# Kernel tuning notes

Measured on AMD Instinct MI355X. Metric: run time of the kernel, lower is better.

The kernel has to match this reference:

```python
import jax, jax.numpy as jnp
import numpy as np

N, E, L, HID, HEADS, G = 50000, 800000, 2, 128, 8, 256
DK = HID // HEADS

def _ln(x, g, b, eps=1e-5):
    m = jnp.mean(x, axis=-1, keepdims=True)
    v = jnp.mean((x - m) ** 2, axis=-1, keepdims=True)
    return (x - m) * jax.lax.rsqrt(v + eps) * g + b

def setup_inputs() -> dict:
    key = jax.random.key(0)
    ks = jax.random.split(key, 24)
    rn = lambda i, s: (0.05 * jax.random.normal(ks[i], s)).astype(jnp.float32)
    return {
        'node_attr': jax.random.randint(ks[0], (N, 4), 0, 64, dtype=jnp.int32),
        'batch_idx': jnp.sort(jax.random.randint(ks[1], (N,), 0, G, dtype=jnp.int32)),
        'edge_index': jax.random.randint(ks[2], (2, E), 0, N, dtype=jnp.int32),
        'strat_dist': jax.random.randint(ks[3], (E,), 0, 32, dtype=jnp.int32),
        'strat_path': jax.random.randint(ks[4], (E,), 0, 16, dtype=jnp.int32),
        'atom_emb': rn(5, (4, 64, HID)),
        'dist_emb': rn(6, (L, 32, HID)),
        'path_emb': rn(7, (L, 16, HID)),
        'Wq': rn(8, (L, HID, HID)), 'bq': rn(9, (L, HID)),
        'Wk': rn(10, (L, HID, HID)), 'bk': rn(11, (L, HID)),
        'Wv': rn(12, (L, HID, HID)), 'bv': rn(13, (L, HID)),
        'Wa': rn(14, (L, HID, HID)), 'ba': rn(15, (L, HID)),
        'ln1_g': jnp.ones((L, HID), jnp.float32), 'ln1_b': jnp.zeros((L, HID), jnp.float32),
        'Wmid': rn(16, (L, HID, 2 * HID)), 'bmid': rn(17, (L, 2 * HID)),
        'Wo': rn(18, (L, 2 * HID, HID)), 'bo': rn(19, (L, HID)),
        'ln2_g': jnp.ones((L, HID), jnp.float32), 'ln2_b': jnp.zeros((L, HID), jnp.float32),
        'W_out': rn(20, (HID, 1)), 'b_out': jnp.zeros((1,), jnp.float32),
    }

def reference(node_attr, batch_idx, edge_index, strat_dist, strat_path,
              atom_emb, dist_emb, path_emb, Wq, bq, Wk, bk, Wv, bv, Wa, ba,
              ln1_g, ln1_b, Wmid, bmid, Wo, bo, ln2_g, ln2_b, W_out, b_out):
    # node encoder: sum of per-feature embeddings (AtomEncoder style)
    x = sum(atom_emb[f][node_attr[:, f]] for f in range(node_attr.shape[1]))  # [N, HID]
    src, tgt = edge_index[0], edge_index[1]  # j (source), i (target)
    inv_sqrt_dk = np.float32(1.0 / np.sqrt(DK))
    for l in range(L):
        # per-edge gather + relational encodings added to the source vector
        s = x[src] + dist_emb[l][strat_dist] + path_emb[l][strat_path]  # [E, HID]
        t = x[tgt]                                                      # [E, HID]
        q = (t @ Wq[l] + bq[l]).reshape(E, HEADS, DK)
        k = (s @ Wk[l] + bk[l]).reshape(E, HEADS, DK)
        v = (s @ Wv[l] + bv[l]).reshape(E, HEADS, DK)
        scores = jnp.sum(q * k, axis=-1) * inv_sqrt_dk  # [E, HEADS]
        # segment softmax keyed on target node id
        smax = jax.ops.segment_max(scores, tgt, num_segments=N)
        ex = jnp.exp(scores - smax[tgt])
        den = jax.ops.segment_sum(ex, tgt, num_segments=N)
        att = ex / (den[tgt] + 1e-16)                   # [E, HEADS]
        msg = (v * att[:, :, None]).reshape(E, HID)
        aggr = jax.ops.segment_sum(msg, tgt, num_segments=N)  # scatter-add
        # update: attn FFN + residual + LayerNorms (dropout is identity in eval)
        h = _ln(jax.nn.gelu(aggr, approximate=False) @ Wa[l] + ba[l] + x, ln1_g[l], ln1_b[l])
        h2 = jax.nn.gelu(h @ Wmid[l] + bmid[l], approximate=False) @ Wo[l] + bo[l]
        x = _ln(h2 + h, ln2_g[l], ln2_b[l])
    # global mean pool per graph, then readout
    cnt = jax.ops.segment_sum(jnp.ones((N,), x.dtype), batch_idx, num_segments=G)
    pooled = jax.ops.segment_sum(x, batch_idx, num_segments=G) / jnp.maximum(cnt, 1.0)[:, None]
    return pooled @ W_out + b_out
```

## Files before the change

### kernel.cpp

```cpp
#include <hip/hip_runtime.h>
#include <hip/hip_bf16.h>
#include <math.h>
#include <stdint.h>

#define N_NODES 50000
#define N_EDGES 800000
#define HID 128
#define NGRAPH 256
#define NLAYER 2
#define CAP 64

#define BIN_B 196
#define N_PAD (BIN_B * 256)

#define ENC_B 782
#define TKV_B 256
#define PREP1_B (BIN_B + ENC_B + TKV_B)

#define PREP0_B (132 + 782)

typedef __bf16 bf16x8 __attribute__((ext_vector_type(8)));
typedef __bf16 bf16x2 __attribute__((ext_vector_type(2)));
typedef float f32x4 __attribute__((ext_vector_type(4)));
typedef float f32x2 __attribute__((ext_vector_type(2)));

__device__ __forceinline__ float gelu_f(float v) {
    return 0.5f * v * (1.0f + erff(v * 0.70710678118654752f));
}

__device__ __forceinline__ f32x2 f8lo(uint32_t d) {
    return __builtin_amdgcn_cvt_pk_f32_fp8((int)d, false);
}
__device__ __forceinline__ f32x2 f8hi(uint32_t d) {
    return __builtin_amdgcn_cvt_pk_f32_fp8((int)d, true);
}
__device__ __forceinline__ uint32_t pk4_fp8(float a, float b, float c, float d) {
    int w = __builtin_amdgcn_cvt_pk_fp8_f32(a, b, 0, false);
    w = __builtin_amdgcn_cvt_pk_fp8_f32(c, d, w, true);
    return (uint32_t)w;
}
__device__ __forceinline__ f32x2 bfpair(uint32_t d) {
    f32x2 r;
    r[0] = __uint_as_float(d << 16);
    r[1] = __uint_as_float(d);
    return r;
}

__global__ __launch_bounds__(256) void prep0_kernel(
    const float* __restrict__ Wq, const float* __restrict__ Wa,
    const float* __restrict__ Wmid, const float* __restrict__ Wo,
    const float* __restrict__ Wk, const float* __restrict__ Wv,
    __bf16* __restrict__ wqkvf, __bf16* __restrict__ waf,
    __bf16* __restrict__ wmidf, __bf16* __restrict__ wof,
    const int* __restrict__ batch, const float* __restrict__ bout,
    const float* __restrict__ bq, const float* __restrict__ bk,
    const float* __restrict__ bv,
    float* __restrict__ invc, float* __restrict__ outp, float* __restrict__ bqkv,
    const int* __restrict__ src, const int* __restrict__ sd,
    const int* __restrict__ sp, uint32_t* __restrict__ pack) {
    int b = blockIdx.x;
    int tid = threadIdx.x;
    if (b < 128) {
        int u = b * 256 + tid;
        int l = u >> 14, r = u & 16383;
        const float* srcp;
        __bf16* dstp;
        int kg, scol, srcCO;
        if (r < 6144) {
            kg = r / 384;
            int uu = r % 384;
            int sec = uu >> 7, cc = uu & 127;
            scol = ((cc & 15) << 3) | (cc >> 4);
            const float* Ws = (sec == 0) ? Wq : (sec == 1) ? Wk : Wv;
            srcp = Ws + l * 16384;
            srcCO = 128;
            dstp = wqkvf + (size_t)l * 49152 + (size_t)r * 8;
        } else if (r < 8192) {
            int rr = r - 6144;
            kg = rr >> 7;
            int cc = rr & 127;
            scol = ((cc & 15) << 3) | (cc >> 4);
            srcp = Wa + l * 16384;
            srcCO = 128;
            dstp = waf + (size_t)l * 16384 + (size_t)rr * 8;
        } else if (r < 12288) {
            int rr = r - 8192;
            kg = rr >> 8;
            int uu = rr & 255;
            int blk = uu >> 7, cc = uu & 127;
            scol = blk * 128 + (((cc & 15) << 3) | (cc >> 4));
            srcp = Wmid + l * 32768;
            srcCO = 256;
            dstp = wmidf + (size_t)l * 32768 + (size_t)rr * 8;
        } else {
            int rr = r - 12288;
            kg = rr >> 7;
            int cc = rr & 127;
            scol = ((cc & 15) << 3) | (cc >> 4);
            srcp = Wo + l * 32768;
            srcCO = 128;
            dstp = wof + (size_t)l * 32768 + (size_t)rr * 8;
        }
        bf16x8 o;
#pragma unroll
        for (int j = 0; j < 8; j++) o[j] = (__bf16)srcp[(kg * 8 + j) * srcCO + scol];
        *(bf16x8*)dstp = o;
    } else if (b < 132) {
        int sb = b - 128;
        if (sb == 0) {
            int g = tid;
            int lo = 0, hi = N_NODES;
            while (lo < hi) { int mid = (lo + hi) >> 1; if (batch[mid] < g) lo = mid + 1; else hi = mid; }
            int start = lo;
            lo = start; hi = N_NODES;
            while (lo < hi) { int mid = (lo + hi) >> 1; if (batch[mid] < g + 1) lo = mid + 1; else hi = mid; }
            int c2 = lo - start;
            invc[g] = 1.0f / fmaxf((float)c2, 1.0f);
            outp[g] = bout[0];
        } else {
            int r = (sb - 1) * 256 + tid;
            int l = r / 384, c = r % 384;
            float v = (c < 128) ? bq[l * 128 + c]
                    : (c < 256) ? bk[l * 128 + c - 128]
                                : bv[l * 128 + c - 256];
            bqkv[r] = v;
        }
    } else {
        int e0 = (b - 132) * 1024 + tid * 4;
        if (e0 + 3 < N_EDGES) {
            int4 s4 = *(const int4*)(src + e0);
            int4 d4 = *(const int4*)(sd + e0);
            int4 p4 = *(const int4*)(sp + e0);
            uint4 o;
            o.x = (uint32_t)s4.x | ((uint32_t)((d4.x << 4) | p4.x) << 16);
            o.y = (uint32_t)s4.y | ((uint32_t)((d4.y << 4) | p4.y) << 16);
            o.z = (uint32_t)s4.z | ((uint32_t)((d4.z << 4) | p4.z) << 16);
            o.w = (uint32_t)s4.w | ((uint32_t)((d4.w << 4) | p4.w) << 16);
            *(uint4*)(pack + e0) = o;
        }
    }
}

__global__ __launch_bounds__(1024) void prep1_kernel(
    const int* __restrict__ attr, const float* __restrict__ aemb,
    __bf16* __restrict__ xb,
    const float* __restrict__ de, const float* __restrict__ pe,
    const float* __restrict__ Wk, const float* __restrict__ Wv,
    __bf16* __restrict__ tkv,
    const int* __restrict__ tgt, const uint32_t* __restrict__ pack,
    int* __restrict__ cnt, uint32_t* __restrict__ ei) {
    __shared__ int lcnt[256];
    __shared__ uint32_t lei[256 * CAP];
    __shared__ float sde[4][128];
    int b = blockIdx.x;
    int tid = threadIdx.x;
    if (b < BIN_B) {
        int lo = b << 8;
        if (tid < 256) lcnt[tid] = 0;
        __syncthreads();
        for (int it0 = 0; it0 < 192; it0 += 4) {
            int4 t4[4];
#pragma unroll
            for (int u = 0; u < 4; u++)
                t4[u] = *(const int4*)(tgt + (it0 + u) * 4096 + tid * 4);
#pragma unroll
            for (int u = 0; u < 4; u++) {
                int e0 = (it0 + u) * 4096 + tid * 4;
#pragma unroll
                for (int j = 0; j < 4; j++) {
                    int t = (j == 0) ? t4[u].x : (j == 1) ? t4[u].y : (j == 2) ? t4[u].z : t4[u].w;
                    unsigned tl = (unsigned)(t - lo);
                    if (tl < 256u) {
                        int r = atomicAdd(&lcnt[tl], 1);
                        if (r < CAP) lei[(tl << 6) + r] = pack[e0 + j];
                    }
                }
            }
        }
        for (int it = 192; it < 196; ++it) {
            int e0 = it * 4096 + tid * 4;
            if (e0 + 3 < N_EDGES) {
                int4 tg = *(const int4*)(tgt + e0);
#pragma unroll
                for (int j = 0; j < 4; j++) {
                    int t = (j == 0) ? tg.x : (j == 1) ? tg.y : (j == 2) ? tg.z : tg.w;
                    unsigned tl = (unsigned)(t - lo);
                    if (tl < 256u) {
                        int r = atomicAdd(&lcnt[tl], 1);
                        if (r < CAP) lei[(tl << 6) + r] = pack[e0 + j];
                    }
                }
            }
        }
        __syncthreads();
        if (tid < 256) {
            int t = lo + tid;
            if (t < N_NODES) cnt[t] = min(lcnt[tid], CAP);
        }
        uint32_t* gout = ei + ((size_t)lo << 6);
#pragma unroll
        for (int i2 = 0; i2 < 4; ++i2) {
            int w = i2 * 4096 + tid * 4;
            *(uint4*)(gout + w) = *(const uint4*)(lei + w);
        }
        return;
    }
    b -= BIN_B;
    if (b < ENC_B) {
        int gid = b * 1024 + tid;
        if (gid < N_NODES * 16) {
            int n = gid >> 4;
            int c8 = (gid & 15) << 3;
            const int4 a = *(const int4*)(attr + n * 4);
            const float* r0 = aemb + (size_t)(0 * 64 + a.x) * 128 + c8;
            const float* r1 = aemb + (size_t)(1 * 64 + a.y) * 128 + c8;
            const float* r2 = aemb + (size_t)(2 * 64 + a.z) * 128 + c8;
            const float* r3 = aemb + (size_t)(3 * 64 + a.w) * 128 + c8;
            f32x4 v0a = *(const f32x4*)r0, v0b = *(const f32x4*)(r0 + 4);
            f32x4 v1a = *(const f32x4*)r1, v1b = *(const f32x4*)(r1 + 4);
            f32x4 v2a = *(const f32x4*)r2, v2b = *(const f32x4*)(r2 + 4);
            f32x4 v3a = *(const f32x4*)r3, v3b = *(const f32x4*)(r3 + 4);
            bf16x8 o;
#pragma unroll
            for (int j = 0; j < 4; j++) {
                o[j] = (__bf16)(v0a[j] + v1a[j] + v2a[j] + v3a[j]);
                o[4 + j] = (__bf16)(v0b[j] + v1b[j] + v2b[j] + v3b[j]);
            }
            *(bf16x8*)(xb + (size_t)n * 128 + c8) = o;
        }
    } else {
        int bb = (b - ENC_B) * 4 + (tid >> 8);
        int c = tid & 255;
        int l = bb >> 9;
        int md = bb & 511;
        int dd = md >> 4, pp = md & 15;
        int g = tid >> 8;
        if (c < 128) sde[g][c] = de[l * 4096 + dd * 128 + c] + pe[l * 2048 + pp * 128 + c];
        __syncthreads();
        const float* W = (c < 128) ? (Wk + l * 16384) : (Wv + l * 16384);
        int cc = c & 127;
        float acc = 0.f;
#pragma unroll 4
        for (int k = 0; k < 128; k++) acc = fmaf(sde[g][k], W[k * 128 + cc], acc);
        tkv[(size_t)bb * 256 + c] = (__bf16)acc;
    }
}

__global__ __launch_bounds__(256) void qkv_gemm(
    const __bf16* __restrict__ A, const __bf16* __restrict__ Wf,
    const float* __restrict__ bias, __bf16* __restrict__ Qb,
    uint8_t* __restrict__ kv8, int M) {
    int tid = threadIdx.x;
    int bq = blockIdx.x;
    int sec = bq % 3;
    int rowblk = bq / 3;
    int lane = tid & 63;
    int wv = tid >> 6;
    int row0 = rowblk * 64 + wv * 16;
    int col0 = sec * 128;
    if (row0 >= M) return;
    int quad = lane >> 4, tq = lane & 15;
    f32x4 acc[8] = {};
#pragma unroll
    for (int k0 = 0; k0 < 128; k0 += 32) {
        int rr = row0 + tq;
        if (rr >= M) rr = M - 1;
        bf16x8 af = *(const bf16x8*)(A + (size_t)rr * 128 + k0 + quad * 8);
#pragma unroll
        for (int nt = 0; nt < 8; nt++) {
            bf16x8 bfr = *(const bf16x8*)(Wf + ((size_t)((k0 >> 3) + quad) * 384 + col0 + nt * 16 + tq) * 8);
            acc[nt] = __builtin_amdgcn_mfma_f32_16x16x32_bf16(af, bfr, acc[nt], 0, 0, 0);
        }
    }
    int cb = tq * 8;
    float bia[8];
#pragma unroll
    for (int t = 0; t < 8; t++) bia[t] = bias[col0 + cb + t];
#pragma unroll
    for (int v = 0; v < 4; v++) {
        int rr = row0 + quad * 4 + v;
        if (rr >= M) continue;
        float val[8];
#pragma unroll
        for (int t = 0; t < 8; t++) val[t] = acc[t][v] + bia[t];
        if (sec == 0) {
            bf16x8 ov;
#pragma unroll
            for (int t = 0; t < 8; t++) ov[t] = (__bf16)val[t];
            *(bf16x8*)(Qb + (size_t)rr * 128 + cb) = ov;
        } else {
            uint2 st;
            st.x = pk4_fp8(val[0], val[1], val[2], val[3]);
            st.y = pk4_fp8(val[4], val[5], val[6], val[7]);
            *(uint2*)(kv8 + (size_t)rr * 256 + (sec - 1) * 128 + cb) = st;
        }
    }
}

template <bool POOL>
__global__ __launch_bounds__(256) void ffn_uber(
    const __bf16* __restrict__ A,
    const __bf16* __restrict__ xres,
    const __bf16* __restrict__ Waf, const float* __restrict__ ba,
    const float* __restrict__ l1g, const float* __restrict__ l1b,
    const __bf16* __restrict__ Wmf, const float* __restrict__ bmid,
    const __bf16* __restrict__ Wof, const float* __restrict__ bo,
    const float* __restrict__ l2g, const float* __restrict__ l2b,
    __bf16* __restrict__ outx,
    const int* __restrict__ batch, const float* __restrict__ invc,
    const float* __restrict__ WoutV, float* __restrict__ outp,
    int M) {
    __shared__ __bf16 hld[4][16][136];
    __shared__ __bf16 smid[4][16][264];
    __shared__ float ps[POOL ? NGRAPH : 1];
    int lane = threadIdx.x & 63;
    int wv = threadIdx.x >> 6;
    int row0 = blockIdx.x * 64 + wv * 16;
    bool active = row0 < M;
    if (POOL) {
        ps[threadIdx.x] = 0.f;
        __syncthreads();
    } else if (!active) {
        return;
    }
    int quad = lane >> 4, tq = lane & 15;
    if (active) {
        int cb = tq * 8;
        {
            f32x4 acc[8] = {};
#pragma unroll
            for (int k0 = 0; k0 < 128; k0 += 32) {
                int rr = row0 + tq;
                if (rr >= M) rr = M - 1;
                bf16x8 af = *(const bf16x8*)(A + (size_t)rr * 128 + k0 + quad * 8);
#pragma unroll
                for (int nt = 0; nt < 8; nt++) {
                    bf16x8 bfr = *(const bf16x8*)(Waf + ((size_t)((k0 >> 3) + quad) * 128 + nt * 16 + tq) * 8);
                    acc[nt] = __builtin_amdgcn_mfma_f32_16x16x32_bf16(af, bfr, acc[nt], 0, 0, 0);
                }
            }
            float bia[8], gv[8], bv2[8];
#pragma unroll
            for (int t = 0; t < 8; t++) {
                bia[t] = ba[cb + t];
                gv[t] = l1g[cb + t];
                bv2[t] = l1b[cb + t];
            }
#pragma unroll
            for (int v = 0; v < 4; v++) {
                int rr = row0 + quad * 4 + v;
                int rc = (rr < M) ? rr : M - 1;
                bf16x8 rv = *(const bf16x8*)(xres + (size_t)rc * 128 + cb);
                float val[8];
#pragma unroll
                for (int t = 0; t < 8; t++) val[t] = acc[t][v] + bia[t] + (float)rv[t];
                float s = 0.f, s2 = 0.f;
#pragma unroll
                for (int t = 0; t < 8; t++) { s += val[t]; s2 = fmaf(val[t], val[t], s2); }
#pragma unroll
                for (int o = 1; o < 16; o <<= 1) {
                    s += __shfl_xor(s, o);
                    s2 += __shfl_xor(s2, o);
                }
                float m = s * (1.0f / 128.0f);
                float var = s2 * (1.0f / 128.0f) - m * m;
                float rs = rsqrtf(var + 1e-5f);
                bf16x8 ov;
#pragma unroll
                for (int t = 0; t < 8; t++) ov[t] = (__bf16)((val[t] - m) * rs * gv[t] + bv2[t]);
                *(bf16x8*)(&hld[wv][quad * 4 + v][cb]) = ov;
            }
        }
        asm volatile("" ::: "memory");
#pragma unroll
        for (int cH = 0; cH < 2; ++cH) {
            f32x4 acc[8] = {};
#pragma unroll
            for (int k0 = 0; k0 < 128; k0 += 32) {
                bf16x8 af = *(const bf16x8*)(&hld[wv][tq][k0 + quad * 8]);
#pragma unroll
                for (int nt = 0; nt < 8; nt++) {
                    bf16x8 bfr = *(const bf16x8*)(Wmf + ((size_t)((k0 >> 3) + quad) * 256 + cH * 128 + nt * 16 + tq) * 8);
                    acc[nt] = __builtin_amdgcn_mfma_f32_16x16x32_bf16(af, bfr, acc[nt], 0, 0, 0);
                }
            }
            int cb2 = cH * 128 + cb;
            float bia[8];
#pragma unroll
            for (int t = 0; t < 8; t++) bia[t] = bmid[cb2 + t];
#pragma unroll
            for (int v = 0; v < 4; v++) {
                bf16x8 ov;
#pragma unroll
                for (int t = 0; t < 8; t++) ov[t] = (__bf16)gelu_f(acc[t][v] + bia[t]);
                *(bf16x8*)(&smid[wv][quad * 4 + v][cb2]) = ov;
            }
        }
        asm volatile("" ::: "memory");
        f32x4 acc[8] = {};
#pragma unroll
        for (int k0 = 0; k0 < 256; k0 += 32) {
            bf16x8 af = *(const bf16x8*)(&smid[wv][tq][k0 + quad * 8]);
#pragma unroll
            for (int nt = 0; nt < 8; nt++) {
                bf16x8 bfr = *(const bf16x8*)(Wof + ((size_t)((k0 >> 3) + quad) * 128 + nt * 16 + tq) * 8);
                acc[nt] = __builtin_amdgcn_mfma_f32_16x16x32_bf16(af, bfr, acc[nt], 0, 0, 0);
            }
        }
        float bia[8], gv[8], bv2[8], wo8[8];
#pragma unroll
        for (int t = 0; t < 8; t++) {
            bia[t] = bo[cb + t];
            gv[t] = l2g[cb + t];
            bv2[t] = l2b[cb + t];
        }
        if (POOL) {
#pragma unroll
            for (int t = 0; t < 8; t++) wo8[t] = WoutV[cb + t];
        }
#pragma unroll
        for (int v = 0; v < 4; v++) {
            int rr = row0 + quad * 4 + v;
            bf16x8 rv = *(const bf16x8*)(&hld[wv][quad * 4 + v][cb]);
            float val[8];
#pragma unroll
            for (int t = 0; t < 8; t++) val[t] = acc[t][v] + bia[t] + (float)rv[t];
            float s = 0.f, s2 = 0.f;
#pragma unroll
            for (int t = 0; t < 8; t++) { s += val[t]; s2 = fmaf(val[t], val[t], s2); }
#pragma unroll
            for (int o = 1; o < 16; o <<= 1) {
                s += __shfl_xor(s, o);
                s2 += __shfl_xor(s2, o);
            }
            float m = s * (1.0f / 128.0f);
            float var = s2 * (1.0f / 128.0f) - m * m;
            float rs = rsqrtf(var + 1e-5f);
#pragma unroll
            for (int t = 0; t < 8; t++) val[t] = (val[t] - m) * rs * gv[t] + bv2[t];
            if (rr >= M) continue;
            if (!POOL) {
                bf16x8 ov;
#pragma unroll
                for (int t = 0; t < 8; t++) ov[t] = (__bf16)val[t];
                *(bf16x8*)(outx + (size_t)rr * 128 + cb) = ov;
            } else {
                float dot = 0.f;
#pragma unroll
                for (int t = 0; t < 8; t++) dot = fmaf(val[t], wo8[t], dot);
#pragma unroll
                for (int o = 1; o < 16; o <<= 1) dot += __shfl_xor(dot, o);
                if (tq == 0) {
                    int g = batch[rr];
                    atomicAdd(&ps[g], dot * invc[g]);
                }
            }
        }
    }
    if (POOL) {
        __syncthreads();
        float pv = ps[threadIdx.x];
        if (pv != 0.f) atomicAdd(&outp[threadIdx.x], pv);
    }
}

__global__ __launch_bounds__(256) void attn_kernel(
    const __bf16* __restrict__ Qb, const uint8_t* __restrict__ kv8,
    const __bf16* __restrict__ tkv,
    const int* __restrict__ cnt, const uint32_t* __restrict__ ei,
    __bf16* __restrict__ outb) {
    __shared__ float red[4][1376];
    int wv = threadIdx.x >> 6;
    int i = blockIdx.x * 4 + wv;
    int lane = threadIdx.x & 63;
    int slot = lane >> 3, h = lane & 7;
    int ch0 = h * 16;
    const uint4* qv = (const uint4*)(Qb + (size_t)i * 128 + ch0);
    uint4 qa = qv[0], qb = qv[1];
    uint32_t qd[8] = {qa.x, qa.y, qa.z, qa.w, qb.x, qb.y, qb.z, qb.w};
    f32x2 qp[8];
#pragma unroll
    for (int j = 0; j < 8; j++) qp[j] = bfpair(qd[j]);
    int deg = cnt[i];
    if (deg > CAP) deg = CAP;
    int p0 = i << 6;
    int p1 = p0 + deg;
    float l = 0.f;
    f32x2 ap[8] = {};
    int p = p0 + slot;
    uint32_t w1 = 0, w2 = 0;
    if (p < p1) w1 = ei[p];
    if (p + 8 < p1) w2 = ei[p + 8];
    uint4 kw, vw, t0, t1, u0, u1;
    {
        int j = w1 & 0xffff, md = w1 >> 16;
        const uint8_t* kr = kv8 + (size_t)j * 256 + ch0;
        kw = *(const uint4*)kr;
        vw = *(const uint4*)(kr + 128);
        const __bf16* tr = tkv + md * 256 + ch0;
        t0 = *(const uint4*)tr;
        t1 = *(const uint4*)(tr + 8);
        u0 = *(const uint4*)(tr + 128);
        u1 = *(const uint4*)(tr + 136);
    }
    while (p < p1) {
        uint4 kwn, vwn, t0n, t1n, u0n, u1n;
        {
            int j = w2 & 0xffff, md = w2 >> 16;
            const uint8_t* kr = kv8 + (size_t)j * 256 + ch0;
            kwn = *(const uint4*)kr;
            vwn = *(const uint4*)(kr + 128);
            const __bf16* tr = tkv + md * 256 + ch0;
            t0n = *(const uint4*)tr;
            t1n = *(const uint4*)(tr + 8);
            u0n = *(const uint4*)(tr + 128);
            u1n = *(const uint4*)(tr + 136);
        }
        int pn = p + 16;
        uint32_t w3 = ei[(pn < p1) ? pn : p];
        uint32_t kd[4] = {kw.x, kw.y, kw.z, kw.w};
        uint32_t vd[4] = {vw.x, vw.y, vw.z, vw.w};
        uint32_t td[8] = {t0.x, t0.y, t0.z, t0.w, t1.x, t1.y, t1.z, t1.w};
        uint32_t ud[8] = {u0.x, u0.y, u0.z, u0.w, u1.x, u1.y, u1.z, u1.w};
        f32x2 sa = {0.f, 0.f};
#pragma unroll
        for (int j = 0; j < 4; j++) {
            f32x2 klo = f8lo(kd[j]) + bfpair(td[2 * j]);
            f32x2 khi = f8hi(kd[j]) + bfpair(td[2 * j + 1]);
            sa = qp[2 * j] * klo + sa;
            sa = qp[2 * j + 1] * khi + sa;
        }
        float s = sa[0] + sa[1];
        float pe = __expf(s * 0.25f);
        l += pe;
        f32x2 pp = {pe, pe};
#pragma unroll
        for (int j = 0; j < 4; j++) {
            f32x2 vlo = f8lo(vd[j]) + bfpair(ud[2 * j]);
            f32x2 vhi = f8hi(vd[j]) + bfpair(ud[2 * j + 1]);
            ap[2 * j] = pp * vlo + ap[2 * j];
            ap[2 * j + 1] = pp * vhi + ap[2 * j + 1];
        }
        kw = kwn; vw = vwn; t0 = t0n; t1 = t1n; u0 = u0n; u1 = u1n;
        w2 = w3;
        p += 8;
    }
    float* rw = red[wv] + slot * 172 + 20 * h;
#pragma unroll
    for (int j = 0; j < 8; j++) *(f32x2*)(rw + 2 * j) = ap[j];
    red[wv][slot * 172 + 156 + h] = l;
    asm volatile("" ::: "memory");
    int pc = 2 * lane + 4 * (lane >> 3);
    int hh = lane >> 3;
    float s0 = 0.f, s1 = 0.f, ls = 0.f;
#pragma unroll
    for (int s = 0; s < 8; s++) {
        float2 v = *(const float2*)(red[wv] + s * 172 + pc);
        s0 += v.x;
        s1 += v.y;
        ls += red[wv][s * 172 + 156 + hh];
    }
    float inv = 1.0f / (ls + 1e-16f);
    bf16x2 o2;
    o2[0] = (__bf16)gelu_f(s0 * inv);
    o2[1] = (__bf16)gelu_f(s1 * inv);
    *(bf16x2*)(outb + (size_t)i * 128 + 2 * lane) = o2;
}

extern "C" void kernel_launch(void* const* d_in, const int* in_sizes, int n_in,
                              void* d_out, int out_size, void* d_ws, size_t ws_size,
                              hipStream_t stream) {
    const int N = N_NODES, E = N_EDGES;
    const int* node_attr = (const int*)d_in[0];
    const int* batch_idx = (const int*)d_in[1];
    const int* edge_index = (const int*)d_in[2];
    const int* strat_dist = (const int*)d_in[3];
    const int* strat_path = (const int*)d_in[4];
    const float* atom_emb = (const float*)d_in[5];
    const float* dist_emb = (const float*)d_in[6];
    const float* path_emb = (const float*)d_in[7];
    const float* Wq = (const float*)d_in[8];
    const float* bq = (const float*)d_in[9];
    const float* Wk = (const float*)d_in[10];
    const float* bk = (const float*)d_in[11];
    const float* Wv = (const float*)d_in[12];
    const float* bv = (const float*)d_in[13];
    const float* Wa = (const float*)d_in[14];
    const float* ba = (const float*)d_in[15];
    const float* ln1g = (const float*)d_in[16];
    const float* ln1b = (const float*)d_in[17];
    const float* Wmid = (const float*)d_in[18];
    const float* bmid = (const float*)d_in[19];
    const float* Wo = (const float*)d_in[20];
    const float* bo = (const float*)d_in[21];
    const float* ln2g = (const float*)d_in[22];
    const float* ln2b = (const float*)d_in[23];
    const float* Wout = (const float*)d_in[24];
    const float* bout = (const float*)d_in[25];
    float* out = (float*)d_out;

    const int* src = edge_index;
    const int* tgt = edge_index + E;

    size_t NF = (size_t)N * HID;
    float* invc = (float*)d_ws;
    float* bqkv = invc + 256;
    __bf16* xb = (__bf16*)(bqkv + 768);
    __bf16* Qb = xb + NF;
    __bf16* ab = Qb + NF;
    __bf16* tkv = ab + NF;
    __bf16* wqkvf = tkv + 262144;
    __bf16* waf = wqkvf + 98304;
    __bf16* wmidf = waf + 32768;
    __bf16* wof = wmidf + 65536;
    uint8_t* kv8 = (uint8_t*)(wof + 65536);
    uint32_t* ei = (uint32_t*)(kv8 + (size_t)N * 256);
    uint32_t* pack = ei + (size_t)N_PAD * CAP;
    int* cnt = (int*)(pack + N_EDGES);

    prep0_kernel<<<PREP0_B, 256, 0, stream>>>(
        Wq, Wa, Wmid, Wo, Wk, Wv, wqkvf, waf, wmidf, wof,
        batch_idx, bout, bq, bk, bv, invc, out, bqkv,
        src, strat_dist, strat_path, pack);
    prep1_kernel<<<PREP1_B, 1024, 0, stream>>>(
        node_attr, atom_emb, xb, dist_emb, path_emb, Wk, Wv, tkv,
        tgt, pack, cnt, ei);

    const int GB = (N + 63) / 64;
    const int AB = (N + 3) / 4;

    for (int l = 0; l < NLAYER; ++l) {
        qkv_gemm<<<3 * GB, 256, 0, stream>>>(
            xb, wqkvf + l * 49152, bqkv + l * 384, Qb, kv8, N);

        attn_kernel<<<AB, 256, 0, stream>>>(Qb, kv8, tkv + l * 131072, cnt, ei, ab);

        if (l < NLAYER - 1) {
            ffn_uber<false><<<GB, 256, 0, stream>>>(
                ab, xb, waf + l * 16384, ba + l * 128, ln1g + l * 128, ln1b + l * 128,
                wmidf + l * 32768, bmid + l * 256, wof + l * 32768, bo + l * 128,
                ln2g + l * 128, ln2b + l * 128, xb,
                nullptr, nullptr, nullptr, nullptr, N);
        } else {
            ffn_uber<true><<<GB, 256, 0, stream>>>(
                ab, xb, waf + l * 16384, ba + l * 128, ln1g + l * 128, ln1b + l * 128,
                wmidf + l * 32768, bmid + l * 256, wof + l * 32768, bo + l * 128,
                ln2g + l * 128, ln2b + l * 128, nullptr,
                batch_idx, invc, Wout, out, N);
        }
    }
}
```

Baseline: 430.6 us.

## Pack edge targets to 16-bit and bin 512 nodes per block

The prep0 pass now also writes a 16-bit copy of the edge target indices, which works because node ids fit in 16 bits. The binning blocks in prep1 read this compact array and each cover 512 target nodes instead of 256, so there are half as many blocks. Since every binning block scans the full edge list, this cuts total target-index read traffic by roughly four times. In exchange, each block does twice the shared-memory atomics and needs about 132KB of LDS, which limits residency to one block per CU. prep0 also gains an extra read and write pass over the target indices.

```diff
diff --git a/kernel.cpp b/kernel.cpp
--- a/kernel.cpp
+++ b/kernel.cpp
@@ -10,8 +10,9 @@
 #define NLAYER 2
 #define CAP 64
 
-#define BIN_B 196
-#define N_PAD (BIN_B * 256)
+#define BIN_B 98
+#define BIN_T 512
+#define N_PAD (BIN_B * BIN_T)
 
 #define ENC_B 782
 #define TKV_B 256
@@ -57,7 +58,8 @@
     const float* __restrict__ bv,
     float* __restrict__ invc, float* __restrict__ outp, float* __restrict__ bqkv,
     const int* __restrict__ src, const int* __restrict__ sd,
-    const int* __restrict__ sp, uint32_t* __restrict__ pack) {
+    const int* __restrict__ sp, const int* __restrict__ tgt,
+    uint32_t* __restrict__ pack, uint16_t* __restrict__ t16) {
     int b = blockIdx.x;
     int tid = threadIdx.x;
     if (b < 128) {
@@ -131,12 +133,17 @@
             int4 s4 = *(const int4*)(src + e0);
             int4 d4 = *(const int4*)(sd + e0);
             int4 p4 = *(const int4*)(sp + e0);
+            int4 t4 = *(const int4*)(tgt + e0);
             uint4 o;
             o.x = (uint32_t)s4.x | ((uint32_t)((d4.x << 4) | p4.x) << 16);
             o.y = (uint32_t)s4.y | ((uint32_t)((d4.y << 4) | p4.y) << 16);
             o.z = (uint32_t)s4.z | ((uint32_t)((d4.z << 4) | p4.z) << 16);
             o.w = (uint32_t)s4.w | ((uint32_t)((d4.w << 4) | p4.w) << 16);
             *(uint4*)(pack + e0) = o;
+            uint2 tt;
+            tt.x = (uint32_t)t4.x | ((uint32_t)t4.y << 16);
+            tt.y = (uint32_t)t4.z | ((uint32_t)t4.w << 16);
+            *(uint2*)(t16 + e0) = tt;
         }
     }
 }
@@ -147,59 +154,69 @@
     const float* __restrict__ de, const float* __restrict__ pe,
     const float* __restrict__ Wk, const float* __restrict__ Wv,
     __bf16* __restrict__ tkv,
-    const int* __restrict__ tgt, const uint32_t* __restrict__ pack,
+    const uint16_t* __restrict__ t16, const uint32_t* __restrict__ pack,
     int* __restrict__ cnt, uint32_t* __restrict__ ei) {
-    __shared__ int lcnt[256];
-    __shared__ uint32_t lei[256 * CAP];
+    __shared__ int lcnt[BIN_T];
+    __shared__ uint32_t lei[BIN_T * CAP];
     __shared__ float sde[4][128];
     int b = blockIdx.x;
     int tid = threadIdx.x;
     if (b < BIN_B) {
-        int lo = b << 8;
-        if (tid < 256) lcnt[tid] = 0;
+        unsigned lo = (unsigned)(b << 9);
+        if (tid < BIN_T) lcnt[tid] = 0;
         __syncthreads();
-        for (int it0 = 0; it0 < 192; it0 += 4) {
-            int4 t4[4];
+        for (int it0 = 0; it0 < 96; it0 += 4) {
+            uint4 w4[4];
 #pragma unroll
             for (int u = 0; u < 4; u++)
-                t4[u] = *(const int4*)(tgt + (it0 + u) * 4096 + tid * 4);
+                w4[u] = *(const uint4*)(t16 + (it0 + u) * 8192 + tid * 8);
 #pragma unroll
             for (int u = 0; u < 4; u++) {
-                int e0 = (it0 + u) * 4096 + tid * 4;
+                int e0 = (it0 + u) * 8192 + tid * 8;
+                uint32_t dws[4] = {w4[u].x, w4[u].y, w4[u].z, w4[u].w};
 #pragma unroll
                 for (int j = 0; j < 4; j++) {
-                    int t = (j == 0) ? t4[u].x : (j == 1) ? t4[u].y : (j == 2) ? t4[u].z : t4[u].w;
-                    unsigned tl = (unsigned)(t - lo);
-                    if (tl < 256u) {
-                        int r = atomicAdd(&lcnt[tl], 1);
-                        if (r < CAP) lei[(tl << 6) + r] = pack[e0 + j];
+                    unsigned ta = (dws[j] & 0xffffu) - lo;
+                    unsigned tb = (dws[j] >> 16) - lo;
+                    if (ta < (unsigned)BIN_T) {
+                        int r = atomicAdd(&lcnt[ta], 1);
+                        if (r < CAP) lei[(ta << 6) + r] = pack[e0 + 2 * j];
+                    }
+                    if (tb < (unsigned)BIN_T) {
+                        int r = atomicAdd(&lcnt[tb], 1);
+                        if (r < CAP) lei[(tb << 6) + r] = pack[e0 + 2 * j + 1];
                     }
                 }
             }
         }
-        for (int it = 192; it < 196; ++it) {
-            int e0 = it * 4096 + tid * 4;
-            if (e0 + 3 < N_EDGES) {
-                int4 tg = *(const int4*)(tgt + e0);
+        for (int it = 96; it < 98; ++it) {
+            int e0 = it * 8192 + tid * 8;
+            if (e0 + 7 < N_EDGES) {
+                uint4 w = *(const uint4*)(t16 + e0);
+                uint32_t dws[4] = {w.x, w.y, w.z, w.w};
 #pragma unroll
                 for (int j = 0; j < 4; j++) {
-                    int t = (j == 0) ? tg.x : (j == 1) ? tg.y : (j == 2) ? tg.z : tg.w;
-                    unsigned tl = (unsigned)(t - lo);
-                    if (tl < 256u) {
-                        int r = atomicAdd(&lcnt[tl], 1);
-                        if (r < CAP) lei[(tl << 6) + r] = pack[e0 + j];
+                    unsigned ta = (dws[j] & 0xffffu) - lo;
+                    unsigned tb = (dws[j] >> 16) - lo;
+                    if (ta < (unsigned)BIN_T) {
+                        int r = atomicAdd(&lcnt[ta], 1);
+                        if (r < CAP) lei[(ta << 6) + r] = pack[e0 + 2 * j];
+                    }
+                    if (tb < (unsigned)BIN_T) {
+                        int r = atomicAdd(&lcnt[tb], 1);
+                        if (r < CAP) lei[(tb << 6) + r] = pack[e0 + 2 * j + 1];
                     }
                 }
             }
         }
         __syncthreads();
-        if (tid < 256) {
-            int t = lo + tid;
+        if (tid < BIN_T) {
+            int t = (int)lo + tid;
             if (t < N_NODES) cnt[t] = min(lcnt[tid], CAP);
         }
         uint32_t* gout = ei + ((size_t)lo << 6);
 #pragma unroll
-        for (int i2 = 0; i2 < 4; ++i2) {
+        for (int i2 = 0; i2 < 8; ++i2) {
             int w = i2 * 4096 + tid * 4;
             *(uint4*)(gout + w) = *(const uint4*)(lei + w);
         }
@@ -617,14 +634,15 @@
     uint32_t* ei = (uint32_t*)(kv8 + (size_t)N * 256);
     uint32_t* pack = ei + (size_t)N_PAD * CAP;
     int* cnt = (int*)(pack + N_EDGES);
+    uint16_t* t16 = (uint16_t*)(cnt + N_NODES);
 
     prep0_kernel<<<PREP0_B, 256, 0, stream>>>(
         Wq, Wa, Wmid, Wo, Wk, Wv, wqkvf, waf, wmidf, wof,
         batch_idx, bout, bq, bk, bv, invc, out, bqkv,
-        src, strat_dist, strat_path, pack);
+        src, strat_dist, strat_path, tgt, pack, t16);
     prep1_kernel<<<PREP1_B, 1024, 0, stream>>>(
         node_attr, atom_emb, xb, dist_emb, path_emb, Wk, Wv, tkv,
-        tgt, pack, cnt, ei);
+        t16, pack, cnt, ei);
 
     const int GB = (N + 63) / 64;
     const int AB = (N + 3) / 4;
```

New measurement: 473.7 us. 1.1x slower.
